# Kernel tuning notes

Measured on AMD Instinct MI355X. Metric: run time of the kernel, lower is better.

The kernel has to match this reference:

```python
import jax, jax.numpy as jnp
import numpy as np

N_NODES = 50000
N_EDGES = 800000


def _gat_conv(x, src, dst, W, att_src, att_dst, bias, heads, out_ch, concat, num_nodes):
    # x: [N, d_in]; W: [d_in, heads*out_ch]; att_*: [heads, out_ch]; bias: [heads*out_ch] or [out_ch]
    xh = (x @ W).reshape(num_nodes, heads, out_ch)          # [N, H, C]
    a_src = jnp.einsum('nhc,hc->nh', xh, att_src)            # [N, H]
    a_dst = jnp.einsum('nhc,hc->nh', xh, att_dst)            # [N, H]
    e = jax.nn.leaky_relu(a_src[src] + a_dst[dst], 0.2)      # [E, H]
    # segment softmax over incoming edges per destination node
    m = jax.ops.segment_max(e, dst, num_segments=num_nodes)  # [N, H]
    ex = jnp.exp(e - m[dst])                                  # [E, H]
    denom = jax.ops.segment_sum(ex, dst, num_segments=num_nodes)  # [N, H]
    coeff = ex / denom[dst]                                   # [E, H]
    # scatter-add aggregation of attention-weighted source features
    out = jax.ops.segment_sum(coeff[:, :, None] * xh[src], dst, num_segments=num_nodes)  # [N, H, C]
    if concat:
        out = out.reshape(num_nodes, heads * out_ch)
    else:
        out = out.mean(axis=1)
    return out + bias


def setup_inputs() -> dict:
    key = jax.random.key(0)
    ks = jax.random.split(key, 10)
    d_in, h1, heads, d_out = 64, 64, 4, 128
    X = jax.random.normal(ks[0], (N_NODES, d_in), dtype=jnp.float32)
    edge_index = jax.random.randint(ks[1], (2, N_EDGES), 0, N_NODES, dtype=jnp.int32)
    s1 = 1.0 / np.sqrt(d_in)
    s2 = 1.0 / np.sqrt(heads * h1)
    return {
        'X': X,
        'edge_index': edge_index,
        'W1': jax.random.normal(ks[2], (d_in, heads * h1), dtype=jnp.float32) * s1,
        'att_src1': jax.random.normal(ks[3], (heads, h1), dtype=jnp.float32) * s2,
        'att_dst1': jax.random.normal(ks[4], (heads, h1), dtype=jnp.float32) * s2,
        'b1': jnp.zeros((heads * h1,), dtype=jnp.float32),
        'W2': jax.random.normal(ks[5], (heads * h1, d_out), dtype=jnp.float32) * s2,
        'att_src2': jax.random.normal(ks[6], (1, d_out), dtype=jnp.float32) * 0.1,
        'att_dst2': jax.random.normal(ks[7], (1, d_out), dtype=jnp.float32) * 0.1,
        'b2': jnp.zeros((d_out,), dtype=jnp.float32),
    }


def reference(X, edge_index, W1, att_src1, att_dst1, b1, W2, att_src2, att_dst2, b2):
    num_nodes = X.shape[0]
    loops = jnp.arange(num_nodes, dtype=edge_index.dtype)
    src = jnp.concatenate([edge_index[0], loops])  # add_self_loops=True
    dst = jnp.concatenate([edge_index[1], loops])
    H = _gat_conv(X, src, dst, W1, att_src1, att_dst1, b1, heads=4, out_ch=64, concat=True, num_nodes=num_nodes)
    H = _gat_conv(H, src, dst, W2, att_src2, att_dst2, b2, heads=1, out_ch=128, concat=False, num_nodes=num_nodes)
    return H
```

## Files before the change

### kernel.cpp

```cpp
#include <hip/hip_runtime.h>
#include <hip/hip_bf16.h>
#include <hip/hip_fp16.h>

typedef float v4 __attribute__((ext_vector_type(4)));
typedef _Float16 hv8 __attribute__((ext_vector_type(8)));
typedef _Float16 h2 __attribute__((ext_vector_type(2)));
typedef unsigned int u32x4 __attribute__((ext_vector_type(4)));
typedef unsigned short u16x4 __attribute__((ext_vector_type(4)));

#define BCAP 8192
#define NCAP 64

__device__ __forceinline__ unsigned short f2h(float f) {
    _Float16 h = (_Float16)f;
    return __builtin_bit_cast(unsigned short, h);
}
__device__ __forceinline__ void unph8(uint4 u, v4& lo, v4& hi) {
    h2 a = __builtin_bit_cast(h2, u.x);
    h2 b = __builtin_bit_cast(h2, u.y);
    h2 c = __builtin_bit_cast(h2, u.z);
    h2 d = __builtin_bit_cast(h2, u.w);
    lo[0] = (float)a[0]; lo[1] = (float)a[1]; lo[2] = (float)b[0]; lo[3] = (float)b[1];
    hi[0] = (float)c[0]; hi[1] = (float)c[1]; hi[2] = (float)d[0]; hi[3] = (float)d[1];
}
__device__ __forceinline__ float leaky02(float x) { return x >= 0.f ? x : 0.2f * x; }


__global__ __launch_bounds__(256) void conv_init_kernel(
    const float* __restrict__ X, const float* __restrict__ W1, const float* __restrict__ W2,
    const float* __restrict__ as1, const float* __restrict__ ad1,
    unsigned short* __restrict__ Xh, unsigned short* __restrict__ W1T,
    unsigned short* __restrict__ W2T, float* __restrict__ vsrc, float* __restrict__ vdst,
    int* __restrict__ bucketCnt,
    int XB, int NX)
{
    int b = blockIdx.x, t = threadIdx.x;
    if (b < XB) {
        int i = (b * 256 + t) * 8;
        if (i < NX) {
            float4 a = *(const float4*)&X[i];
            float4 c = *(const float4*)&X[i + 4];
            ushort4 r0; r0.x = f2h(a.x); r0.y = f2h(a.y); r0.z = f2h(a.z); r0.w = f2h(a.w);
            ushort4 r1; r1.x = f2h(c.x); r1.y = f2h(c.y); r1.z = f2h(c.z); r1.w = f2h(c.w);
            *(ushort4*)&Xh[i] = r0;
            *(ushort4*)&Xh[i + 4] = r1;
        }
    } else if (b < XB + 64) {
        int id = (b - XB) * 256 + t;
        int j = id >> 6, k = id & 63;
        W1T[id] = f2h(W1[k * 256 + j]);
    } else if (b < XB + 64 + 128) {
        int id = (b - XB - 64) * 256 + t;
        int j = id >> 8, k = id & 255;
        W2T[id] = f2h(W2[k * 128 + j]);
    } else if (b == XB + 64 + 128) {
        bucketCnt[t] = 0;
    } else {
        int vb = b - (XB + 64 + 128 + 1);
        const float* att = vb ? ad1 : as1;
        float* vout = vb ? vdst : vsrc;
        int h = t >> 6, k = t & 63;
        float s = 0.f;
        const float* wrow = &W1[k * 256 + h * 64];
        const float* arow = &att[h * 64];
        #pragma unroll 8
        for (int c = 0; c < 64; c++) s += wrow[c] * arow[c];
        vout[t] = s;
    }
}


__global__ __launch_bounds__(256) void bin_att_kernel(
    const int* __restrict__ src, const int* __restrict__ dst,
    int* __restrict__ bucketCnt, unsigned* __restrict__ binned,
    const unsigned short* __restrict__ Xh, const float* __restrict__ vsrc,
    const float* __restrict__ vdst, float* __restrict__ a_src1, float* __restrict__ a_dst1,
    int E, int T, int BINB, int N)
{
    int t = threadIdx.x;
    if ((int)blockIdx.x < BINB) {
        __shared__ int cnt[256];
        __shared__ int basep[256];
        cnt[t] = 0; __syncthreads();
        int base = blockIdx.x * 2048;
        unsigned pv[8]; int bk[8], rv[8];
        #pragma unroll
        for (int j = 0; j < 8; j++) {
            int id = base + j * 256 + t;
            if (id < T) {
                int ss, dd;
                if (id < E) { ss = src[id]; dd = dst[id]; }
                else        { ss = dd = id - E; }
                bk[j] = dd >> 8;
                pv[j] = ((unsigned)(dd & 255) << 24) | (unsigned)ss;
                rv[j] = atomicAdd(&cnt[bk[j]], 1);
            } else bk[j] = -1;
        }
        __syncthreads();
        int v = cnt[t];
        if (v) basep[t] = t * BCAP + atomicAdd(&bucketCnt[t], v);
        __syncthreads();
        #pragma unroll
        for (int j = 0; j < 8; j++) {
            if (bk[j] >= 0)
                binned[basep[bk[j]] + rv[j]] = pv[j];
        }
    } else {
        __shared__ float vs[256], vd[256];
        vs[t] = vsrc[t]; vd[t] = vdst[t];
        __syncthreads();
        int w = t >> 6, lane = t & 63;
        int nd = lane >> 3, sub = lane & 7, kc = sub * 8;
        int node = (blockIdx.x - BINB) * 32 + w * 8 + nd;
        if (node >= N) node = N - 1;
        uint4 x = *(const uint4*)&Xh[(size_t)node * 64 + kc];
        v4 lo, hi; unph8(x, lo, hi);
        float ps[4], pd[4];
        #pragma unroll
        for (int h = 0; h < 4; h++) {
            float s = 0.f, d = 0.f;
            #pragma unroll
            for (int j = 0; j < 4; j++) {
                s += lo[j] * vs[h * 64 + kc + j];     d += lo[j] * vd[h * 64 + kc + j];
                s += hi[j] * vs[h * 64 + kc + 4 + j]; d += hi[j] * vd[h * 64 + kc + 4 + j];
            }
            ps[h] = s; pd[h] = d;
        }
        #pragma unroll
        for (int off = 1; off < 8; off <<= 1)
            #pragma unroll
            for (int h = 0; h < 4; h++) {
                ps[h] += __shfl_xor(ps[h], off);
                pd[h] += __shfl_xor(pd[h], off);
            }
        if (sub == 0) {
            v4 o0; o0[0] = ps[0]; o0[1] = ps[1]; o0[2] = ps[2]; o0[3] = ps[3];
            v4 o1; o1[0] = pd[0]; o1[1] = pd[1]; o1[2] = pd[2]; o1[3] = pd[3];
            *(v4*)&a_src1[node * 4] = o0;
            *(v4*)&a_dst1[node * 4] = o1;
        }
    }
}


__global__ __launch_bounds__(256) void place_kernel(
    const int* __restrict__ bucketCnt, const unsigned* __restrict__ binned,
    int* __restrict__ counts, int* __restrict__ csr_src, int N)
{
    __shared__ int cur[256];
    int b = blockIdx.x, t = threadIdx.x;
    cur[t] = 0; __syncthreads();
    int beg = b * BCAP, end = beg + bucketCnt[b];
    int nb0 = b * 256;
    for (int i = beg + t; i < end; i += 256) {
        unsigned u = binned[i];
        int dl = u >> 24;
        int s  = (int)(u & 0xFFFFFF);
        int r = atomicAdd(&cur[dl], 1);
        if (r < NCAP) csr_src[(size_t)(nb0 + dl) * NCAP + r] = s;
    }
    __syncthreads();
    int n = nb0 + t;
    if (n < N) {
        int c = cur[t]; if (c > NCAP) c = NCAP;
        counts[n] = c;
        int cp = (c + 7) & ~7;
        size_t o = (size_t)n * NCAP;
        for (int q = c; q < cp; q++) csr_src[o + q] = n;
    }
}


__global__ __launch_bounds__(256) void aggX_kernel(
    const int* __restrict__ counts, const int* __restrict__ csr_src,
    const float* __restrict__ a_src1, const float* __restrict__ a_dst1,
    const unsigned short* __restrict__ Xh, unsigned short* __restrict__ Xagg, int N)
{
    __shared__ float wlds[4][2][64][4];
    __shared__ int   slds[4][2][64];
    int wid  = threadIdx.x >> 6;
    int lane = threadIdx.x & 63;
    int nd = lane >> 5;
    int hl = lane & 31;
    int p = (lane >> 3) & 3, sub = lane & 7, kc = sub * 8;
    int n = blockIdx.x * 8 + wid * 2 + nd;
    if (n >= N) return;
    int cnt  = counts[n];
    int degp = (cnt + 7) & ~7;
    size_t beg = (size_t)n * NCAP;
    int L = degp;
    v4 adst = *(const v4*)&a_dst1[n * 4];
    float (*wn)[4] = wlds[wid][nd];
    int* sn = slds[wid][nd];

    v4 den = (v4)0.f;
    for (int q = hl; q < L; q += 32) {
        int s = __builtin_nontemporal_load(&csr_src[beg + q]);
        v4 a = *(const v4*)&a_src1[s * 4];
        v4 wv;
        #pragma unroll
        for (int h = 0; h < 4; h++) {
            float e = fminf(leaky02(a[h] + adst[h]), 80.f);
            wv[h] = (q < cnt) ? __expf(e) : 0.f;
        }
        *(v4*)wn[q] = wv;
        sn[q] = s;
        den += wv;
    }
    #pragma unroll
    for (int off = 1; off < 32; off <<= 1)
        #pragma unroll
        for (int h = 0; h < 4; h++) den[h] += __shfl_xor(den[h], off);

    v4 accL[4], accH[4];
    #pragma unroll
    for (int h = 0; h < 4; h++) { accL[h] = (v4)0.f; accH[h] = (v4)0.f; }

    int steps = L >> 2;
    auto sidx = [&](int i) { int j = i < steps ? i : steps - 1; return j * 4 + p; };
    int sa_ = sn[sidx(0)], sb_ = sn[sidx(1)];
    uint4 xa = *(const uint4*)&Xh[(size_t)sa_ * 64 + kc];
    uint4 xb = *(const uint4*)&Xh[(size_t)sb_ * 64 + kc];
    for (int i = 0; i < steps; i++) {
        int sc_ = sn[sidx(i + 2)];
        uint4 xc = *(const uint4*)&Xh[(size_t)sc_ * 64 + kc];
        v4 w = *(const v4*)wn[i * 4 + p];
        v4 lo, hi; unph8(xa, lo, hi);
        #pragma unroll
        for (int h = 0; h < 4; h++) { accL[h] += w[h] * lo; accH[h] += w[h] * hi; }
        xa = xb; xb = xc;
    }

    #pragma unroll
    for (int off = 8; off < 32; off <<= 1) {
        #pragma unroll
        for (int h = 0; h < 4; h++) {
            #pragma unroll
            for (int c = 0; c < 4; c++) {
                accL[h][c] += __shfl_xor(accL[h][c], off);
                accH[h][c] += __shfl_xor(accH[h][c], off);
            }
        }
    }
    if (p == 0) {
        #pragma unroll
        for (int h = 0; h < 4; h++) {
            float inv = 1.f / den[h];
            v4 oL = accL[h] * inv, oH = accH[h] * inv;
            u32x4 pk;
            pk[0] = (unsigned)f2h(oL[0]) | ((unsigned)f2h(oL[1]) << 16);
            pk[1] = (unsigned)f2h(oL[2]) | ((unsigned)f2h(oL[3]) << 16);
            pk[2] = (unsigned)f2h(oH[0]) | ((unsigned)f2h(oH[1]) << 16);
            pk[3] = (unsigned)f2h(oH[2]) | ((unsigned)f2h(oH[3]) << 16);
            __builtin_nontemporal_store(pk, (u32x4*)&Xagg[(size_t)n * 256 + h * 64 + kc]);
        }
    }
}


__global__ __launch_bounds__(256) void gemmHW2_kernel(
    const unsigned short* __restrict__ Xagg, const unsigned short* __restrict__ W1T,
    const float* __restrict__ b1, const unsigned short* __restrict__ W2T,
    const float* __restrict__ att_src, const float* __restrict__ att_dst,
    unsigned short* __restrict__ xh2, float* __restrict__ a_src2, float* __restrict__ a_dst2,
    int N)
{
    __shared__ unsigned short As[64 * 264];
    __shared__ unsigned short Ws[256 * 72];
    int t  = threadIdx.x;
    int n0 = blockIdx.x * 64;
    int w = t >> 6, l = t & 63;
    int quad = l >> 4, lm = l & 15;

    #pragma unroll
    for (int c = 0; c < 8; c++) {
        int idx = c * 256 + t;
        int row = idx >> 5, seg = idx & 31;
        int gr = n0 + row; if (gr >= N) gr = N - 1;
        *(uint4*)&As[row * 264 + seg * 8] = *(const uint4*)&Xagg[(size_t)gr * 256 + seg * 8];
    }
    #pragma unroll
    for (int c = 0; c < 8; c++) {
        int idx = c * 256 + t;
        int row = idx >> 3, seg = idx & 7;
        *(uint4*)&Ws[row * 72 + seg * 8] = *(const uint4*)&W1T[row * 64 + seg * 8];
    }
    __syncthreads();

    v4 hacc[2][8];
    #pragma unroll
    for (int r = 0; r < 2; r++) {
        int tl = w * 2 + r;
        int nq = tl & 3, th = tl >> 2;
        hv8 xf0[2], xf1[2];
        #pragma unroll
        for (int hh = 0; hh < 2; hh++) {
            int h = th * 2 + hh;
            xf0[hh] = *(const hv8*)&As[(nq * 16 + lm) * 264 + h * 64 + quad * 8];
            xf1[hh] = *(const hv8*)&As[(nq * 16 + lm) * 264 + h * 64 + 32 + quad * 8];
        }
        #pragma unroll
        for (int tt2 = 0; tt2 < 8; tt2++) {
            int tt = th * 8 + tt2;
            int hh = tt2 >> 2;
            hv8 wf0 = *(const hv8*)&Ws[(tt * 16 + lm) * 72 + quad * 8];
            hv8 wf1 = *(const hv8*)&Ws[(tt * 16 + lm) * 72 + 32 + quad * 8];
            v4 a = (v4)0.f;
            a = __builtin_amdgcn_mfma_f32_16x16x32_f16(wf0, xf0[hh], a, 0, 0, 0);
            a = __builtin_amdgcn_mfma_f32_16x16x32_f16(wf1, xf1[hh], a, 0, 0, 0);
            int ch = tt * 16 + quad * 4;
            v4 bias = *(const v4*)&b1[ch];
            hacc[r][tt2] = a + bias;
        }
    }
    __syncthreads();
    #pragma unroll
    for (int r = 0; r < 2; r++) {
        int tl = w * 2 + r;
        int nq = tl & 3, th = tl >> 2;
        #pragma unroll
        for (int tt2 = 0; tt2 < 8; tt2++) {
            int tt = th * 8 + tt2;
            int ch = tt * 16 + quad * 4;
            v4 o = hacc[r][tt2];
            u16x4 b;
            b[0] = f2h(o[0]); b[1] = f2h(o[1]); b[2] = f2h(o[2]); b[3] = f2h(o[3]);
            *(u16x4*)&As[(nq * 16 + lm) * 264 + ch] = b;
        }
    }

    v4 acc[8];
    #pragma unroll
    for (int tt = 0; tt < 8; tt++) acc[tt] = (v4)0.f;
    for (int kt = 0; kt < 256; kt += 64) {
        __syncthreads();
        #pragma unroll
        for (int c = 0; c < 4; c++) {
            int idx = c * 256 + t;
            int row = idx >> 3, seg = idx & 7;
            *(uint4*)&Ws[row * 72 + seg * 8] = *(const uint4*)&W2T[row * 256 + kt + seg * 8];
        }
        __syncthreads();

        hv8 xf0 = *(const hv8*)&As[(w * 16 + lm) * 264 + kt + quad * 8];
        hv8 xf1 = *(const hv8*)&As[(w * 16 + lm) * 264 + kt + 32 + quad * 8];
        #pragma unroll
        for (int tt = 0; tt < 8; tt++) {
            hv8 wf0 = *(const hv8*)&Ws[(tt * 16 + lm) * 72 + quad * 8];
            hv8 wf1 = *(const hv8*)&Ws[(tt * 16 + lm) * 72 + 32 + quad * 8];
            acc[tt] = __builtin_amdgcn_mfma_f32_16x16x32_f16(wf0, xf0, acc[tt], 0, 0, 0);
            acc[tt] = __builtin_amdgcn_mfma_f32_16x16x32_f16(wf1, xf1, acc[tt], 0, 0, 0);
        }
    }

    int node = n0 + w * 16 + lm;
    float vs = 0.f, vd = 0.f;
    #pragma unroll
    for (int tt = 0; tt < 8; tt++) {
        int ch = tt * 16 + quad * 4;
        v4 d = acc[tt];
        v4 as_ = *(const v4*)&att_src[ch];
        v4 ad_ = *(const v4*)&att_dst[ch];
        #pragma unroll
        for (int r = 0; r < 4; r++) { vs += d[r] * as_[r]; vd += d[r] * ad_[r]; }
        ushort4 b; b.x = f2h(d[0]); b.y = f2h(d[1]); b.z = f2h(d[2]); b.w = f2h(d[3]);
        if (node < N) *(ushort4*)&xh2[(size_t)node * 128 + ch] = b;
    }
    vs += __shfl_xor(vs, 16); vs += __shfl_xor(vs, 32);
    vd += __shfl_xor(vd, 16); vd += __shfl_xor(vd, 32);
    if (l < 16 && node < N) { a_src2[node] = vs; a_dst2[node] = vd; }
}


__global__ __launch_bounds__(256) void aggf2_kernel(
    const int* __restrict__ counts, const int* __restrict__ csr_src,
    const float* __restrict__ a_src2, const float* __restrict__ a_dst2,
    const unsigned short* __restrict__ xh2, const float* __restrict__ b2,
    float* __restrict__ out, int N)
{
    __shared__ float wlds[4][2][64];
    __shared__ int   slds[4][2][64];
    int wid  = threadIdx.x >> 6;
    int lane = threadIdx.x & 63;
    int nd = lane >> 5;
    int hl = lane & 31;
    int p = (lane >> 4) & 1;
    int c0 = (lane & 15) * 8;
    int n = blockIdx.x * 8 + wid * 2 + nd;
    if (n >= N) return;
    int cnt  = counts[n];
    int degp = (cnt + 7) & ~7;
    size_t beg = (size_t)n * NCAP;
    int L = degp;
    float adst = a_dst2[n];
    float* wn = wlds[wid][nd];
    int*   sn = slds[wid][nd];

    float den = 0.f;
    for (int q = hl; q < L; q += 32) {
        int s = __builtin_nontemporal_load(&csr_src[beg + q]);
        float a = a_src2[s];
        float e = fminf(leaky02(a + adst), 80.f);
        float w = (q < cnt) ? __expf(e) : 0.f;
        wn[q] = w; sn[q] = s;
        den += w;
    }
    #pragma unroll
    for (int off = 1; off < 32; off <<= 1) den += __shfl_xor(den, off);

    v4 accL = (v4)0.f, accH = (v4)0.f;
    int steps = L >> 1;
    auto sidx = [&](int i) { int j = i < steps ? i : steps - 1; return j * 2 + p; };
    int sa_ = sn[sidx(0)], sb_ = sn[sidx(1)];
    uint4 xa = *(const uint4*)&xh2[(size_t)sa_ * 128 + c0];
    uint4 xb = *(const uint4*)&xh2[(size_t)sb_ * 128 + c0];
    for (int i = 0; i < steps; i++) {
        int sc_ = sn[sidx(i + 2)];
        uint4 xc = *(const uint4*)&xh2[(size_t)sc_ * 128 + c0];
        float w = wn[i * 2 + p];
        v4 lo, hi; unph8(xa, lo, hi);
        accL += w * lo; accH += w * hi;
        xa = xb; xb = xc;
    }

    #pragma unroll
    for (int c = 0; c < 4; c++) {
        accL[c] += __shfl_xor(accL[c], 16);
        accH[c] += __shfl_xor(accH[c], 16);
    }
    if (p == 0) {
        float inv = 1.f / den;
        v4 bl = *(const v4*)&b2[c0];
        v4 bh = *(const v4*)&b2[c0 + 4];
        v4 oL = accL * inv + bl;
        v4 oH = accH * inv + bh;
        __builtin_nontemporal_store(oL, (v4*)&out[(size_t)n * 128 + c0]);
        __builtin_nontemporal_store(oH, (v4*)&out[(size_t)n * 128 + c0 + 4]);
    }
}


static inline size_t rnd256(size_t x) { return (x + 255) & ~(size_t)255; }

extern "C" void kernel_launch(void* const* d_in, const int* in_sizes, int n_in,
                              void* d_out, int out_size, void* d_ws, size_t ws_size,
                              hipStream_t stream) {
    const float* X   = (const float*)d_in[0];
    const int*   ei  = (const int*)d_in[1];
    const float* W1  = (const float*)d_in[2];
    const float* as1 = (const float*)d_in[3];
    const float* ad1 = (const float*)d_in[4];
    const float* b1  = (const float*)d_in[5];
    const float* W2  = (const float*)d_in[6];
    const float* as2 = (const float*)d_in[7];
    const float* ad2 = (const float*)d_in[8];
    const float* b2  = (const float*)d_in[9];
    float* out = (float*)d_out;

    const int N = in_sizes[0] / 64;
    const int E = in_sizes[1] / 2;
    const int T = E + N;
    const int NBUK = (N + 255) >> 8;
    const int* srcArr = ei;
    const int* dstArr = ei + E;
    const int XB = (N * 64 / 8 + 255) / 256;
    const int BINB = (T + 2047) / 2048;
    const int ATTB = (N + 31) / 32;

    char* w = (char*)d_ws;
    unsigned short* Xh     = (unsigned short*)w;  w += rnd256((size_t)N * 64 * 2);
    unsigned short* W1T    = (unsigned short*)w;  w += rnd256((size_t)256 * 64 * 2);
    unsigned short* W2T    = (unsigned short*)w;  w += rnd256((size_t)128 * 256 * 2);
    float* vsrc    = (float*)w;  w += rnd256(256 * 4);
    float* vdst    = (float*)w;  w += rnd256(256 * 4);
    unsigned short* Xagg   = (unsigned short*)w;  w += rnd256((size_t)N * 256 * 2);
    unsigned short* xh2    = (unsigned short*)w;  w += rnd256((size_t)N * 128 * 2);
    float* a_src1  = (float*)w;  w += rnd256((size_t)N * 4 * 4);
    float* a_dst1  = (float*)w;  w += rnd256((size_t)N * 4 * 4);
    float* a_src2v = (float*)w;  w += rnd256((size_t)N * 4);
    float* a_dst2v = (float*)w;  w += rnd256((size_t)N * 4);
    int*   counts  = (int*)w;    w += rnd256((size_t)N * 4);
    int*   bucketCnt = (int*)w;  w += rnd256(256 * 4);
    unsigned* binned = (unsigned*)w; w += rnd256((size_t)NBUK * BCAP * 4);
    int*   csr_src = (int*)w;    w += rnd256((size_t)NBUK * 256 * NCAP * 4);

    conv_init_kernel<<<XB + 64 + 128 + 1 + 2, 256, 0, stream>>>(
        X, W1, W2, as1, ad1, Xh, W1T, W2T, vsrc, vdst, bucketCnt, XB, N * 64);
    bin_att_kernel<<<BINB + ATTB, 256, 0, stream>>>(srcArr, dstArr, bucketCnt, binned,
                                                    Xh, vsrc, vdst, a_src1, a_dst1,
                                                    E, T, BINB, N);
    place_kernel<<<NBUK, 256, 0, stream>>>(bucketCnt, binned, counts, csr_src, N);
    aggX_kernel<<<(N + 7) / 8, 256, 0, stream>>>(counts, csr_src, a_src1, a_dst1,
                                                 Xh, Xagg, N);
    gemmHW2_kernel<<<(N + 63) / 64, 256, 0, stream>>>(Xagg, W1T, b1, W2T, as2, ad2,
                                                      xh2, a_src2v, a_dst2v, N);
    aggf2_kernel<<<(N + 7) / 8, 256, 0, stream>>>(counts, csr_src, a_src2v, a_dst2v,
                                                  xh2, b2, out, N);
}
```

Before: 202.4 us.

## Fuse layer-1 aggregation into GEMM kernel and merge prep kernels

Layer-1 attention aggregation now runs inside the GEMM kernel and writes its fp16 aggregated rows straight into shared memory. This removes the Xagg global round-trip and one kernel launch. The conversion, binning and attention-score kernels are merged into one prep kernel that recomputes the W1·att vectors per block and reads X in fp32, and bucket counters are cleared with a memset. In exchange, the fused kernel has far fewer blocks (one per 64 nodes instead of one per 8), each doing serial gather work before its GEMM, which may lower occupancy and latency hiding. The per-block recomputation of the attention vectors also adds redundant work.

```diff
diff --git a/kernel.cpp b/kernel.cpp
--- a/kernel.cpp
+++ b/kernel.cpp
@@ -26,13 +26,15 @@
 __device__ __forceinline__ float leaky02(float x) { return x >= 0.f ? x : 0.2f * x; }
 
 
-__global__ __launch_bounds__(256) void conv_init_kernel(
+__global__ __launch_bounds__(256) void prep_kernel(
     const float* __restrict__ X, const float* __restrict__ W1, const float* __restrict__ W2,
     const float* __restrict__ as1, const float* __restrict__ ad1,
+    const int* __restrict__ src, const int* __restrict__ dst,
+    int* __restrict__ bucketCnt, unsigned* __restrict__ binned,
     unsigned short* __restrict__ Xh, unsigned short* __restrict__ W1T,
-    unsigned short* __restrict__ W2T, float* __restrict__ vsrc, float* __restrict__ vdst,
-    int* __restrict__ bucketCnt,
-    int XB, int NX)
+    unsigned short* __restrict__ W2T,
+    float* __restrict__ a_src1, float* __restrict__ a_dst1,
+    int XB, int NX, int E, int T, int BINB, int N)
 {
     int b = blockIdx.x, t = threadIdx.x;
     if (b < XB) {
@@ -49,40 +51,15 @@
         int id = (b - XB) * 256 + t;
         int j = id >> 6, k = id & 63;
         W1T[id] = f2h(W1[k * 256 + j]);
-    } else if (b < XB + 64 + 128) {
+    } else if (b < XB + 192) {
         int id = (b - XB - 64) * 256 + t;
         int j = id >> 8, k = id & 255;
         W2T[id] = f2h(W2[k * 128 + j]);
-    } else if (b == XB + 64 + 128) {
-        bucketCnt[t] = 0;
-    } else {
-        int vb = b - (XB + 64 + 128 + 1);
-        const float* att = vb ? ad1 : as1;
-        float* vout = vb ? vdst : vsrc;
-        int h = t >> 6, k = t & 63;
-        float s = 0.f;
-        const float* wrow = &W1[k * 256 + h * 64];
-        const float* arow = &att[h * 64];
-        #pragma unroll 8
-        for (int c = 0; c < 64; c++) s += wrow[c] * arow[c];
-        vout[t] = s;
-    }
-}
-
-
-__global__ __launch_bounds__(256) void bin_att_kernel(
-    const int* __restrict__ src, const int* __restrict__ dst,
-    int* __restrict__ bucketCnt, unsigned* __restrict__ binned,
-    const unsigned short* __restrict__ Xh, const float* __restrict__ vsrc,
-    const float* __restrict__ vdst, float* __restrict__ a_src1, float* __restrict__ a_dst1,
-    int E, int T, int BINB, int N)
-{
-    int t = threadIdx.x;
-    if ((int)blockIdx.x < BINB) {
+    } else if (b < XB + 192 + BINB) {
         __shared__ int cnt[256];
         __shared__ int basep[256];
         cnt[t] = 0; __syncthreads();
-        int base = blockIdx.x * 2048;
+        int base = (b - XB - 192) * 2048;
         unsigned pv[8]; int bk[8], rv[8];
         #pragma unroll
         for (int j = 0; j < 8; j++) {
@@ -107,23 +84,32 @@
         }
     } else {
         __shared__ float vs[256], vd[256];
-        vs[t] = vsrc[t]; vd[t] = vdst[t];
+        {
+            int h = t >> 6, k = t & 63;
+            const float* wrow = &W1[k * 256 + h * 64];
+            const float* ar = &as1[h * 64];
+            const float* dr = &ad1[h * 64];
+            float sv = 0.f, dv = 0.f;
+            #pragma unroll 8
+            for (int c = 0; c < 64; c++) { sv += wrow[c] * ar[c]; dv += wrow[c] * dr[c]; }
+            vs[t] = sv; vd[t] = dv;
+        }
         __syncthreads();
         int w = t >> 6, lane = t & 63;
         int nd = lane >> 3, sub = lane & 7, kc = sub * 8;
-        int node = (blockIdx.x - BINB) * 32 + w * 8 + nd;
+        int node = (b - XB - 192 - BINB) * 32 + w * 8 + nd;
         if (node >= N) node = N - 1;
-        uint4 x = *(const uint4*)&Xh[(size_t)node * 64 + kc];
-        v4 lo, hi; unph8(x, lo, hi);
+        float4 xlo = *(const float4*)&X[(size_t)node * 64 + kc];
+        float4 xhi = *(const float4*)&X[(size_t)node * 64 + kc + 4];
         float ps[4], pd[4];
         #pragma unroll
         for (int h = 0; h < 4; h++) {
-            float s = 0.f, d = 0.f;
-            #pragma unroll
-            for (int j = 0; j < 4; j++) {
-                s += lo[j] * vs[h * 64 + kc + j];     d += lo[j] * vd[h * 64 + kc + j];
-                s += hi[j] * vs[h * 64 + kc + 4 + j]; d += hi[j] * vd[h * 64 + kc + 4 + j];
-            }
+            const float* vsh = &vs[h * 64 + kc];
+            const float* vdh = &vd[h * 64 + kc];
+            float s = xlo.x * vsh[0] + xlo.y * vsh[1] + xlo.z * vsh[2] + xlo.w * vsh[3]
+                    + xhi.x * vsh[4] + xhi.y * vsh[5] + xhi.z * vsh[6] + xhi.w * vsh[7];
+            float d = xlo.x * vdh[0] + xlo.y * vdh[1] + xlo.z * vdh[2] + xlo.w * vdh[3]
+                    + xhi.x * vdh[4] + xhi.y * vdh[5] + xhi.z * vdh[6] + xhi.w * vdh[7];
             ps[h] = s; pd[h] = d;
         }
         #pragma unroll
@@ -171,95 +157,10 @@
 }
 
 
-__global__ __launch_bounds__(256) void aggX_kernel(
+__global__ __launch_bounds__(256) void aggGemm_kernel(
     const int* __restrict__ counts, const int* __restrict__ csr_src,
     const float* __restrict__ a_src1, const float* __restrict__ a_dst1,
-    const unsigned short* __restrict__ Xh, unsigned short* __restrict__ Xagg, int N)
-{
-    __shared__ float wlds[4][2][64][4];
-    __shared__ int   slds[4][2][64];
-    int wid  = threadIdx.x >> 6;
-    int lane = threadIdx.x & 63;
-    int nd = lane >> 5;
-    int hl = lane & 31;
-    int p = (lane >> 3) & 3, sub = lane & 7, kc = sub * 8;
-    int n = blockIdx.x * 8 + wid * 2 + nd;
-    if (n >= N) return;
-    int cnt  = counts[n];
-    int degp = (cnt + 7) & ~7;
-    size_t beg = (size_t)n * NCAP;
-    int L = degp;
-    v4 adst = *(const v4*)&a_dst1[n * 4];
-    float (*wn)[4] = wlds[wid][nd];
-    int* sn = slds[wid][nd];
-
-    v4 den = (v4)0.f;
-    for (int q = hl; q < L; q += 32) {
-        int s = __builtin_nontemporal_load(&csr_src[beg + q]);
-        v4 a = *(const v4*)&a_src1[s * 4];
-        v4 wv;
-        #pragma unroll
-        for (int h = 0; h < 4; h++) {
-            float e = fminf(leaky02(a[h] + adst[h]), 80.f);
-            wv[h] = (q < cnt) ? __expf(e) : 0.f;
-        }
-        *(v4*)wn[q] = wv;
-        sn[q] = s;
-        den += wv;
-    }
-    #pragma unroll
-    for (int off = 1; off < 32; off <<= 1)
-        #pragma unroll
-        for (int h = 0; h < 4; h++) den[h] += __shfl_xor(den[h], off);
-
-    v4 accL[4], accH[4];
-    #pragma unroll
-    for (int h = 0; h < 4; h++) { accL[h] = (v4)0.f; accH[h] = (v4)0.f; }
-
-    int steps = L >> 2;
-    auto sidx = [&](int i) { int j = i < steps ? i : steps - 1; return j * 4 + p; };
-    int sa_ = sn[sidx(0)], sb_ = sn[sidx(1)];
-    uint4 xa = *(const uint4*)&Xh[(size_t)sa_ * 64 + kc];
-    uint4 xb = *(const uint4*)&Xh[(size_t)sb_ * 64 + kc];
-    for (int i = 0; i < steps; i++) {
-        int sc_ = sn[sidx(i + 2)];
-        uint4 xc = *(const uint4*)&Xh[(size_t)sc_ * 64 + kc];
-        v4 w = *(const v4*)wn[i * 4 + p];
-        v4 lo, hi; unph8(xa, lo, hi);
-        #pragma unroll
-        for (int h = 0; h < 4; h++) { accL[h] += w[h] * lo; accH[h] += w[h] * hi; }
-        xa = xb; xb = xc;
-    }
-
-    #pragma unroll
-    for (int off = 8; off < 32; off <<= 1) {
-        #pragma unroll
-        for (int h = 0; h < 4; h++) {
-            #pragma unroll
-            for (int c = 0; c < 4; c++) {
-                accL[h][c] += __shfl_xor(accL[h][c], off);
-                accH[h][c] += __shfl_xor(accH[h][c], off);
-            }
-        }
-    }
-    if (p == 0) {
-        #pragma unroll
-        for (int h = 0; h < 4; h++) {
-            float inv = 1.f / den[h];
-            v4 oL = accL[h] * inv, oH = accH[h] * inv;
-            u32x4 pk;
-            pk[0] = (unsigned)f2h(oL[0]) | ((unsigned)f2h(oL[1]) << 16);
-            pk[1] = (unsigned)f2h(oL[2]) | ((unsigned)f2h(oL[3]) << 16);
-            pk[2] = (unsigned)f2h(oH[0]) | ((unsigned)f2h(oH[1]) << 16);
-            pk[3] = (unsigned)f2h(oH[2]) | ((unsigned)f2h(oH[3]) << 16);
-            __builtin_nontemporal_store(pk, (u32x4*)&Xagg[(size_t)n * 256 + h * 64 + kc]);
-        }
-    }
-}
-
-
-__global__ __launch_bounds__(256) void gemmHW2_kernel(
-    const unsigned short* __restrict__ Xagg, const unsigned short* __restrict__ W1T,
+    const unsigned short* __restrict__ Xh, const unsigned short* __restrict__ W1T,
     const float* __restrict__ b1, const unsigned short* __restrict__ W2T,
     const float* __restrict__ att_src, const float* __restrict__ att_dst,
     unsigned short* __restrict__ xh2, float* __restrict__ a_src2, float* __restrict__ a_dst2,
@@ -269,16 +170,93 @@
     __shared__ unsigned short Ws[256 * 72];
     int t  = threadIdx.x;
     int n0 = blockIdx.x * 64;
-    int w = t >> 6, l = t & 63;
-    int quad = l >> 4, lm = l & 15;
-
-    #pragma unroll
-    for (int c = 0; c < 8; c++) {
-        int idx = c * 256 + t;
-        int row = idx >> 5, seg = idx & 31;
-        int gr = n0 + row; if (gr >= N) gr = N - 1;
-        *(uint4*)&As[row * 264 + seg * 8] = *(const uint4*)&Xagg[(size_t)gr * 256 + seg * 8];
-    }
+    int wid = t >> 6, lane = t & 63;
+    int quad = lane >> 4, lm = lane & 15;
+
+    {
+        int nd = lane >> 5;
+        int hl = lane & 31;
+        int p = (lane >> 3) & 3, sub = lane & 7, kc = sub * 8;
+        float* fb = (float*)Ws;
+        float (*wn)[4] = (float(*)[4])(fb + (wid * 2 + nd) * 256);
+        int*   sn      = (int*)(fb + 2048) + (wid * 2 + nd) * 64;
+
+        for (int it = 0; it < 8; it++) {
+            int lrow = wid * 16 + it * 2 + nd;
+            int n = n0 + lrow;
+            int nc = n < N ? n : N - 1;
+            int cnt  = counts[nc];
+            int degp = (cnt + 7) & ~7;
+            size_t beg = (size_t)nc * NCAP;
+            int L = degp;
+            v4 adst = *(const v4*)&a_dst1[nc * 4];
+
+            v4 den = (v4)0.f;
+            for (int q = hl; q < L; q += 32) {
+                int s = __builtin_nontemporal_load(&csr_src[beg + q]);
+                v4 a = *(const v4*)&a_src1[s * 4];
+                v4 wv;
+                #pragma unroll
+                for (int h = 0; h < 4; h++) {
+                    float e = fminf(leaky02(a[h] + adst[h]), 80.f);
+                    wv[h] = (q < cnt) ? __expf(e) : 0.f;
+                }
+                *(v4*)wn[q] = wv;
+                sn[q] = s;
+                den += wv;
+            }
+            #pragma unroll
+            for (int off = 1; off < 32; off <<= 1)
+                #pragma unroll
+                for (int h = 0; h < 4; h++) den[h] += __shfl_xor(den[h], off);
+
+            v4 accL[4], accH[4];
+            #pragma unroll
+            for (int h = 0; h < 4; h++) { accL[h] = (v4)0.f; accH[h] = (v4)0.f; }
+
+            int steps = L >> 2;
+            auto sidx = [&](int i) { int j = i < steps ? i : steps - 1; return j * 4 + p; };
+            int sa_ = sn[sidx(0)], sb_ = sn[sidx(1)];
+            uint4 xa = *(const uint4*)&Xh[(size_t)sa_ * 64 + kc];
+            uint4 xb = *(const uint4*)&Xh[(size_t)sb_ * 64 + kc];
+            for (int i = 0; i < steps; i++) {
+                int sc_ = sn[sidx(i + 2)];
+                uint4 xc = *(const uint4*)&Xh[(size_t)sc_ * 64 + kc];
+                v4 w = *(const v4*)wn[i * 4 + p];
+                v4 lo, hi; unph8(xa, lo, hi);
+                #pragma unroll
+                for (int h = 0; h < 4; h++) { accL[h] += w[h] * lo; accH[h] += w[h] * hi; }
+                xa = xb; xb = xc;
+            }
+
+            #pragma unroll
+            for (int off = 8; off < 32; off <<= 1) {
+                #pragma unroll
+                for (int h = 0; h < 4; h++) {
+                    #pragma unroll
+                    for (int c = 0; c < 4; c++) {
+                        accL[h][c] += __shfl_xor(accL[h][c], off);
+                        accH[h][c] += __shfl_xor(accH[h][c], off);
+                    }
+                }
+            }
+            if (p == 0) {
+                #pragma unroll
+                for (int h = 0; h < 4; h++) {
+                    float inv = 1.f / den[h];
+                    v4 oL = accL[h] * inv, oH = accH[h] * inv;
+                    u32x4 pk;
+                    pk[0] = (unsigned)f2h(oL[0]) | ((unsigned)f2h(oL[1]) << 16);
+                    pk[1] = (unsigned)f2h(oL[2]) | ((unsigned)f2h(oL[3]) << 16);
+                    pk[2] = (unsigned)f2h(oH[0]) | ((unsigned)f2h(oH[1]) << 16);
+                    pk[3] = (unsigned)f2h(oH[2]) | ((unsigned)f2h(oH[3]) << 16);
+                    *(u32x4*)&As[lrow * 264 + h * 64 + kc] = pk;
+                }
+            }
+        }
+    }
+    __syncthreads();
+
     #pragma unroll
     for (int c = 0; c < 8; c++) {
         int idx = c * 256 + t;
@@ -290,7 +268,7 @@
     v4 hacc[2][8];
     #pragma unroll
     for (int r = 0; r < 2; r++) {
-        int tl = w * 2 + r;
+        int tl = wid * 2 + r;
         int nq = tl & 3, th = tl >> 2;
         hv8 xf0[2], xf1[2];
         #pragma unroll
@@ -316,7 +294,7 @@
     __syncthreads();
     #pragma unroll
     for (int r = 0; r < 2; r++) {
-        int tl = w * 2 + r;
+        int tl = wid * 2 + r;
         int nq = tl & 3, th = tl >> 2;
         #pragma unroll
         for (int tt2 = 0; tt2 < 8; tt2++) {
@@ -342,8 +320,8 @@
         }
         __syncthreads();
 
-        hv8 xf0 = *(const hv8*)&As[(w * 16 + lm) * 264 + kt + quad * 8];
-        hv8 xf1 = *(const hv8*)&As[(w * 16 + lm) * 264 + kt + 32 + quad * 8];
+        hv8 xf0 = *(const hv8*)&As[(wid * 16 + lm) * 264 + kt + quad * 8];
+        hv8 xf1 = *(const hv8*)&As[(wid * 16 + lm) * 264 + kt + 32 + quad * 8];
         #pragma unroll
         for (int tt = 0; tt < 8; tt++) {
             hv8 wf0 = *(const hv8*)&Ws[(tt * 16 + lm) * 72 + quad * 8];
@@ -353,7 +331,7 @@
         }
     }
 
-    int node = n0 + w * 16 + lm;
+    int node = n0 + wid * 16 + lm;
     float vs = 0.f, vd = 0.f;
     #pragma unroll
     for (int tt = 0; tt < 8; tt++) {
@@ -368,7 +346,7 @@
     }
     vs += __shfl_xor(vs, 16); vs += __shfl_xor(vs, 32);
     vd += __shfl_xor(vd, 16); vd += __shfl_xor(vd, 32);
-    if (l < 16 && node < N) { a_src2[node] = vs; a_dst2[node] = vd; }
+    if (lane < 16 && node < N) { a_src2[node] = vs; a_dst2[node] = vd; }
 }
 
 
@@ -471,9 +449,6 @@
     unsigned short* Xh     = (unsigned short*)w;  w += rnd256((size_t)N * 64 * 2);
     unsigned short* W1T    = (unsigned short*)w;  w += rnd256((size_t)256 * 64 * 2);
     unsigned short* W2T    = (unsigned short*)w;  w += rnd256((size_t)128 * 256 * 2);
-    float* vsrc    = (float*)w;  w += rnd256(256 * 4);
-    float* vdst    = (float*)w;  w += rnd256(256 * 4);
-    unsigned short* Xagg   = (unsigned short*)w;  w += rnd256((size_t)N * 256 * 2);
     unsigned short* xh2    = (unsigned short*)w;  w += rnd256((size_t)N * 128 * 2);
     float* a_src1  = (float*)w;  w += rnd256((size_t)N * 4 * 4);
     float* a_dst1  = (float*)w;  w += rnd256((size_t)N * 4 * 4);
@@ -484,15 +459,13 @@
     unsigned* binned = (unsigned*)w; w += rnd256((size_t)NBUK * BCAP * 4);
     int*   csr_src = (int*)w;    w += rnd256((size_t)NBUK * 256 * NCAP * 4);
 
-    conv_init_kernel<<<XB + 64 + 128 + 1 + 2, 256, 0, stream>>>(
-        X, W1, W2, as1, ad1, Xh, W1T, W2T, vsrc, vdst, bucketCnt, XB, N * 64);
-    bin_att_kernel<<<BINB + ATTB, 256, 0, stream>>>(srcArr, dstArr, bucketCnt, binned,
-                                                    Xh, vsrc, vdst, a_src1, a_dst1,
-                                                    E, T, BINB, N);
+    hipMemsetAsync(bucketCnt, 0, 256 * sizeof(int), stream);
+    prep_kernel<<<XB + 192 + BINB + ATTB, 256, 0, stream>>>(
+        X, W1, W2, as1, ad1, srcArr, dstArr, bucketCnt, binned,
+        Xh, W1T, W2T, a_src1, a_dst1, XB, N * 64, E, T, BINB, N);
     place_kernel<<<NBUK, 256, 0, stream>>>(bucketCnt, binned, counts, csr_src, N);
-    aggX_kernel<<<(N + 7) / 8, 256, 0, stream>>>(counts, csr_src, a_src1, a_dst1,
-                                                 Xh, Xagg, N);
-    gemmHW2_kernel<<<(N + 63) / 64, 256, 0, stream>>>(Xagg, W1T, b1, W2T, as2, ad2,
+    aggGemm_kernel<<<(N + 63) / 64, 256, 0, stream>>>(counts, csr_src, a_src1, a_dst1,
+                                                      Xh, W1T, b1, W2T, as2, ad2,
                                                       xh2, a_src2v, a_dst2v, N);
     aggf2_kernel<<<(N + 7) / 8, 256, 0, stream>>>(counts, csr_src, a_src2v, a_dst2v,
                                                   xh2, b2, out, N);
```

Result: slower. 230.9 us (+14.1%).
